# Performance work log

Measured on AMD Instinct MI355X. Metric: run time of the kernel, lower is better.

Reference implementation:

```python
import jax, jax.numpy as jnp
import numpy as np

N, E, NB, P = 100000, 1600000, 1000, 500000


def gcn_conv(x, edge_index, W, b):
    # PyG GCNConv: add self-loops, symmetric D^-1/2 (A+I) D^-1/2 normalization,
    # linear transform, bias.
    n = x.shape[0]
    loop = jnp.arange(n, dtype=edge_index.dtype)
    src = jnp.concatenate([edge_index[0], loop])
    dst = jnp.concatenate([edge_index[1], loop])
    deg = jax.ops.segment_sum(jnp.ones(src.shape[0], x.dtype), dst, num_segments=n)
    dinv = jnp.where(deg > 0, jax.lax.rsqrt(deg), 0.0)
    norm = dinv[src] * dinv[dst]                       # [E+n]
    xw = x @ W                                          # [n, out]
    out = jax.ops.segment_sum(xw[src] * norm[:, None], dst, num_segments=n)
    return out + b


def setup_inputs() -> dict:
    key = jax.random.key(0)
    ks = jax.random.split(key, 12)
    x = jax.random.normal(ks[0], (N, 27), jnp.float32)
    edge_index = jax.random.randint(ks[1], (2, E), 0, N, dtype=jnp.int32)
    bank = jax.random.normal(ks[2], (NB, 27), jnp.float32)
    node1 = jax.random.randint(ks[3], (P,), 0, N + NB, dtype=jnp.int32)
    node2 = jax.random.randint(ks[4], (P,), 0, N + NB, dtype=jnp.int32)

    def lin(k, fan_in, fan_out):
        s = 1.0 / np.sqrt(fan_in)
        kw, kb = jax.random.split(k)
        W = jax.random.uniform(kw, (fan_in, fan_out), jnp.float32, -s, s)
        b = jax.random.uniform(kb, (fan_out,), jnp.float32, -s, s)
        return W, b

    W1, b1 = lin(ks[5], 27, 60)
    W2, b2 = lin(ks[6], 60, 50)
    Wb, bb = lin(ks[7], 27, 50)
    Wf1, bf1 = lin(ks[8], 100, 40)
    Wf2, bf2 = lin(ks[9], 40, 20)
    Wf3, bf3 = lin(ks[10], 20, 4)
    return dict(x=x, bank=bank, W1=W1, b1=b1, W2=W2, b2=b2, Wb=Wb, bb=bb,
                Wf1=Wf1, bf1=bf1, Wf2=Wf2, bf2=bf2, Wf3=Wf3, bf3=bf3,
                edge_index=edge_index, node1=node1, node2=node2)


def reference(x, bank, W1, b1, W2, b2, Wb, bb, Wf1, bf1, Wf2, bf2, Wf3, bf3,
              edge_index, node1, node2):
    h = gcn_conv(x, edge_index, W1, b1)                 # [N, 60]
    h = gcn_conv(h, edge_index, W2, b2)                 # [N, 50]
    bk = bank @ Wb + bb                                 # [NB, 50]
    allh = jnp.concatenate([h, bk], axis=0)             # [N+NB, 50]
    z = jnp.concatenate([allh[node1], allh[node2]], axis=1)  # [P, 100]
    z = z @ Wf1 + bf1
    z = z @ Wf2 + bf2
    z = z @ Wf3 + bf3                                   # [P, 4]
    return jax.nn.softmax(z, axis=0)                    # softmax over dim 0, as in source
```

## Files before the change

### kernel.cpp

```cpp
#include <hip/hip_runtime.h>
#include <math.h>

#define N_NODES 100000
#define N_EDGES 1600000
#define NB_BANK 1000
#define N_PAIRS 500000

#define BUCK_SHIFT 8
#define BUCK_NODES 256
#define NBUCK 391
#define BCAP 5504
#define EPB 4096
#define NSCAT 391
#define NZB4 489
#define SMASK 0x1FFFF

struct Consts {
  float C[27*8];
  float Rb[27*8];
  float u[8];
  float vg[8];
  float vb[8];
};

__device__ void precompute_body(
    const float* __restrict__ W1, const float* __restrict__ b1,
    const float* __restrict__ W2, const float* __restrict__ b2,
    const float* __restrict__ Wb, const float* __restrict__ bb,
    const float* __restrict__ Wf1, const float* __restrict__ bf1,
    const float* __restrict__ Wf2, const float* __restrict__ bf2,
    const float* __restrict__ Wf3, const float* __restrict__ bf3,
    Consts* __restrict__ cst) {
  __shared__ float A[40*4];
  __shared__ float T[100*4];
  __shared__ float B[60*8];
  __shared__ float cvec[4];
  const int tid = threadIdx.x;
  const int nt = blockDim.x;

  for (int idx = tid; idx < 160; idx += nt) {
    int r = idx >> 2, k = idx & 3;
    float s = 0.f;
    for (int j = 0; j < 20; ++j) s += Wf2[r*20+j] * Wf3[j*4+k];
    A[idx] = s;
  }
  __syncthreads();
  for (int idx = tid; idx < 400; idx += nt) {
    int r = idx >> 2, k = idx & 3;
    float s = 0.f;
    for (int j = 0; j < 40; ++j) s += Wf1[r*40+j] * A[j*4+k];
    T[idx] = s;
  }
  if (tid < 4) {
    float s = bf3[tid];
    for (int j = 0; j < 40; ++j) s += bf1[j] * A[j*4+tid];
    for (int j = 0; j < 20; ++j) s += bf2[j] * Wf3[j*4+tid];
    cvec[tid] = s;
  }
  __syncthreads();
  for (int idx = tid; idx < 480; idx += nt) {
    int r = idx >> 3, k = idx & 7;
    int half = k >> 2, kk = k & 3;
    float s = 0.f;
    for (int j = 0; j < 50; ++j) s += W2[r*50+j] * T[(half*50+j)*4+kk];
    B[idx] = s;
  }
  __syncthreads();
  for (int idx = tid; idx < 456; idx += nt) {
    if (idx < 216) {
      int r = idx >> 3, k = idx & 7;
      float s = 0.f;
      for (int j = 0; j < 60; ++j) s += W1[r*60+j] * B[j*8+k];
      cst->C[idx] = s;
    } else if (idx < 432) {
      int i2 = idx - 216;
      int r = i2 >> 3, k = i2 & 7, half = k >> 2, kk = k & 3;
      float s = 0.f;
      for (int j = 0; j < 50; ++j) s += Wb[r*50+j] * T[(half*50+j)*4+kk];
      cst->Rb[i2] = s;
    } else if (idx < 440) {
      int k = idx - 432;
      float s = 0.f;
      for (int j = 0; j < 60; ++j) s += b1[j] * B[j*8+k];
      cst->u[k] = s;
    } else if (idx < 448) {
      int k = idx - 440, half = k >> 2, kk = k & 3;
      float s = (half == 0) ? cvec[kk] : 0.f;
      for (int j = 0; j < 50; ++j) s += b2[j] * T[(half*50+j)*4+kk];
      cst->vg[k] = s;
    } else {
      int k = idx - 448, half = k >> 2, kk = k & 3;
      float s = (half == 0) ? cvec[kk] : 0.f;
      for (int j = 0; j < 50; ++j) s += bb[j] * T[(half*50+j)*4+kk];
      cst->vb[k] = s;
    }
  }
}

__global__ __launch_bounds__(1024) void k_scatter(
    const int* __restrict__ ei, int* __restrict__ bcnt, int* __restrict__ ebuf,
    const float* __restrict__ W1, const float* __restrict__ b1,
    const float* __restrict__ W2, const float* __restrict__ b2,
    const float* __restrict__ Wb, const float* __restrict__ bb,
    const float* __restrict__ Wf1, const float* __restrict__ bf1,
    const float* __restrict__ Wf2, const float* __restrict__ bf2,
    const float* __restrict__ Wf3, const float* __restrict__ bf3,
    Consts* __restrict__ cst) {
  if (blockIdx.x == NSCAT) {
    precompute_body(W1, b1, W2, b2, Wb, bb, Wf1, bf1, Wf2, bf2, Wf3, bf3, cst);
    return;
  }
  __shared__ int hist[NBUCK];
  __shared__ int base[NBUCK];
  const int t = threadIdx.x;
  const int e0 = blockIdx.x * EPB;
  int dcache[EPB / 1024];
  if (t < NBUCK) hist[t] = 0;
  __syncthreads();
#pragma unroll
  for (int i = 0; i < EPB / 1024; ++i) {
    int e = e0 + i * 1024 + t;
    int d = (e < N_EDGES) ? ei[N_EDGES + e] : -1;
    dcache[i] = d;
    if (d >= 0) atomicAdd(&hist[d >> BUCK_SHIFT], 1);
  }
  __syncthreads();
  if (t < NBUCK) {
    int h = hist[t];
    base[t] = h ? (t * BCAP + atomicAdd(&bcnt[t], h)) : 0;
    hist[t] = 0;
  }
  __syncthreads();
#pragma unroll
  for (int i = 0; i < EPB / 1024; ++i) {
    int e = e0 + i * 1024 + t;
    int d = dcache[i];
    if (d >= 0) {
      int s = ei[e];
      int b = d >> BUCK_SHIFT;
      int pos = base[b] + atomicAdd(&hist[b], 1);
      ebuf[pos] = ((d & (BUCK_NODES - 1)) << 17) | s;
    }
  }
}

__global__ __launch_bounds__(512) void k_degfill_x8(
    const int* __restrict__ bcnt, const int* __restrict__ ebuf,
    const float* __restrict__ x, const Consts* __restrict__ cst,
    float* __restrict__ dinv, int* __restrict__ rbeg, int* __restrict__ rend,
    int* __restrict__ csr, float* __restrict__ Xs) {
  __shared__ int cnt[BUCK_NODES];
  __shared__ int lcur[BUCK_NODES];
  __shared__ float sdinv[BUCK_NODES];
  __shared__ float xs[BUCK_NODES * 27];
  const int b = blockIdx.x;
  const int t = threadIdx.x;
  if (t < BUCK_NODES) cnt[t] = 0;
  __syncthreads();
  const int beg = b * BCAP, end = beg + bcnt[b];
  for (int j = beg + t; j < end; j += 512)
    atomicAdd(&cnt[ebuf[j] >> 17], 1);
  const int xbase = b * (BUCK_NODES * 27);
  for (int j = t; j < BUCK_NODES * 27; j += 512) {
    int g = xbase + j;
    xs[j] = (g < N_NODES * 27) ? x[g] : 0.f;
  }
  __syncthreads();
  int v = (t < BUCK_NODES) ? cnt[t] : 0;
  for (int off = 1; off < BUCK_NODES; off <<= 1) {
    int u = (t < BUCK_NODES && t >= off) ? cnt[t - off] : 0;
    __syncthreads();
    if (t < BUCK_NODES) cnt[t] += u;
    __syncthreads();
  }
  if (t < BUCK_NODES) {
    const int node = (b << BUCK_SHIFT) + t;
    const int excl = beg + cnt[t] - v;
    lcur[t] = excl;
    float dv = rsqrtf((float)v + 1.0f);
    sdinv[t] = dv;
    if (node < N_NODES) {
      rbeg[node] = excl;
      rend[node] = excl + v;
      dinv[node] = dv;
    }
  }
  __syncthreads();
  for (int j = beg + t; j < end; j += 512) {
    int code = ebuf[j];
    int pos = atomicAdd(&lcur[code >> 17], 1);
    csr[pos] = code & SMASK;
  }
  for (int idx = t; idx < BUCK_NODES * 8; idx += 512) {
    int li = idx >> 3, k = idx & 7;
    int node = (b << BUCK_SHIFT) + li;
    if (node < N_NODES) {
      float s = 0.f;
      for (int c = 0; c < 27; ++c) s += xs[li*27+c] * cst->C[c*8+k];
      Xs[(size_t)node*8+k] = s * sdinv[li];
    }
  }
}

__global__ __launch_bounds__(256) void k_gather1(const int* __restrict__ rbeg,
                                                 const int* __restrict__ rend,
                                                 const int* __restrict__ csr,
                                                 const float* __restrict__ dinv,
                                                 const float2* __restrict__ Xs2,
                                                 float2* __restrict__ Ys2,
                                                 float* __restrict__ dvec) {
  int t = blockIdx.x * 256 + threadIdx.x;
  int d = t >> 2, q = t & 3;
  if (d >= N_NODES) return;
  const int beg = rbeg[d], end = rend[d];
  const float nd = dinv[d];
  float2 self = Xs2[d*4 + q];
  float ax = self.x, ay = self.y;
  float dsum = nd;
  int j = beg;
  if (j + 8 <= end) {
    int s0 = csr[j],   s1 = csr[j+1], s2 = csr[j+2], s3 = csr[j+3];
    int s4 = csr[j+4], s5 = csr[j+5], s6 = csr[j+6], s7 = csr[j+7];
    for (;;) {
      float2 a0 = Xs2[s0*4+q], a1 = Xs2[s1*4+q], a2 = Xs2[s2*4+q], a3 = Xs2[s3*4+q];
      float2 a4 = Xs2[s4*4+q], a5 = Xs2[s5*4+q], a6 = Xs2[s6*4+q], a7 = Xs2[s7*4+q];
      float d0 = 0.f, d1 = 0.f, d2 = 0.f, d3 = 0.f;
      float d4 = 0.f, d5 = 0.f, d6 = 0.f, d7 = 0.f;
      if (q == 0) {
        d0 = dinv[s0]; d1 = dinv[s1]; d2 = dinv[s2]; d3 = dinv[s3];
        d4 = dinv[s4]; d5 = dinv[s5]; d6 = dinv[s6]; d7 = dinv[s7];
      }
      int jn = j + 8;
      bool more = (jn + 8 <= end);
      int u0, u1, u2, u3, u4, u5, u6, u7;
      if (more) {
        u0 = csr[jn];   u1 = csr[jn+1]; u2 = csr[jn+2]; u3 = csr[jn+3];
        u4 = csr[jn+4]; u5 = csr[jn+5]; u6 = csr[jn+6]; u7 = csr[jn+7];
      } else {
        u0 = u1 = u2 = u3 = u4 = u5 = u6 = u7 = 0;
      }
      ax += ((a0.x + a1.x) + (a2.x + a3.x)) + ((a4.x + a5.x) + (a6.x + a7.x));
      ay += ((a0.y + a1.y) + (a2.y + a3.y)) + ((a4.y + a5.y) + (a6.y + a7.y));
      if (q == 0)
        dsum += ((d0 + d1) + (d2 + d3)) + ((d4 + d5) + (d6 + d7));
      j = jn;
      if (!more) break;
      s0 = u0; s1 = u1; s2 = u2; s3 = u3;
      s4 = u4; s5 = u5; s6 = u6; s7 = u7;
    }
  }
  if (j + 4 <= end) {
    int a = csr[j], b = csr[j+1], c = csr[j+2], e = csr[j+3];
    float2 p0 = Xs2[a*4+q], p1 = Xs2[b*4+q], p2 = Xs2[c*4+q], p3 = Xs2[e*4+q];
    ax += (p0.x + p1.x) + (p2.x + p3.x);
    ay += (p0.y + p1.y) + (p2.y + p3.y);
    if (q == 0) dsum += (dinv[a] + dinv[b]) + (dinv[c] + dinv[e]);
    j += 4;
  }
  for (; j < end; ++j) {
    int s = csr[j];
    float2 a = Xs2[s*4+q];
    ax += a.x; ay += a.y;
    if (q == 0) dsum += dinv[s];
  }
  float nn = nd * nd;
  Ys2[t] = make_float2(nn * ax, nn * ay);
  if (q == 0) dvec[d] = nd * dsum;
}

__global__ __launch_bounds__(256) void k_gather2g(const int* __restrict__ rbeg,
                                                  const int* __restrict__ rend,
                                                  const int* __restrict__ csr,
                                                  const float* __restrict__ dinv,
                                                  const float2* __restrict__ Ys2,
                                                  const float* __restrict__ dvec,
                                                  const float* __restrict__ bank,
                                                  const Consts* __restrict__ cst,
                                                  float2* __restrict__ gall2) {
  int t = blockIdx.x * 256 + threadIdx.x;
  int d = t >> 2, q = t & 3;
  if (d >= N_NODES + NB_BANK) return;
  int c0 = 2*q, c1 = 2*q + 1;
  if (d >= N_NODES) {
    int bk = d - N_NODES;
    float sx = cst->vb[c0], sy = cst->vb[c1];
    for (int cc = 0; cc < 27; ++cc) {
      float bv = bank[bk*27+cc];
      sx += bv * cst->Rb[cc*8+c0];
      sy += bv * cst->Rb[cc*8+c1];
    }
    gall2[t] = make_float2(sx, sy);
    return;
  }
  const int beg = rbeg[d], end = rend[d];
  float2 self = Ys2[d*4 + q];
  float ax = self.x, ay = self.y;
  int j = beg;
  if (j + 8 <= end) {
    int s0 = csr[j],   s1 = csr[j+1], s2 = csr[j+2], s3 = csr[j+3];
    int s4 = csr[j+4], s5 = csr[j+5], s6 = csr[j+6], s7 = csr[j+7];
    for (;;) {
      float2 a0 = Ys2[s0*4+q], a1 = Ys2[s1*4+q], a2 = Ys2[s2*4+q], a3 = Ys2[s3*4+q];
      float2 a4 = Ys2[s4*4+q], a5 = Ys2[s5*4+q], a6 = Ys2[s6*4+q], a7 = Ys2[s7*4+q];
      int jn = j + 8;
      bool more = (jn + 8 <= end);
      int u0, u1, u2, u3, u4, u5, u6, u7;
      if (more) {
        u0 = csr[jn];   u1 = csr[jn+1]; u2 = csr[jn+2]; u3 = csr[jn+3];
        u4 = csr[jn+4]; u5 = csr[jn+5]; u6 = csr[jn+6]; u7 = csr[jn+7];
      } else {
        u0 = u1 = u2 = u3 = u4 = u5 = u6 = u7 = 0;
      }
      ax += ((a0.x + a1.x) + (a2.x + a3.x)) + ((a4.x + a5.x) + (a6.x + a7.x));
      ay += ((a0.y + a1.y) + (a2.y + a3.y)) + ((a4.y + a5.y) + (a6.y + a7.y));
      j = jn;
      if (!more) break;
      s0 = u0; s1 = u1; s2 = u2; s3 = u3;
      s4 = u4; s5 = u5; s6 = u6; s7 = u7;
    }
  }
  if (j + 4 <= end) {
    int a = csr[j], b = csr[j+1], c = csr[j+2], e = csr[j+3];
    float2 p0 = Ys2[a*4+q], p1 = Ys2[b*4+q], p2 = Ys2[c*4+q], p3 = Ys2[e*4+q];
    ax += (p0.x + p1.x) + (p2.x + p3.x);
    ay += (p0.y + p1.y) + (p2.y + p3.y);
    j += 4;
  }
  for (; j < end; ++j) {
    float2 a = Ys2[csr[j]*4+q];
    ax += a.x; ay += a.y;
  }
  float nd = dinv[d], dv = dvec[d];
  gall2[t] = make_float2(nd * ax + dv * cst->u[c0] + cst->vg[c0],
                         nd * ay + dv * cst->u[c1] + cst->vg[c1]);
}

__device__ inline void sm_merge(float4& m1, float4& s1,
                                const float4 m2, const float4 s2) {
  float4 M;
  M.x = fmaxf(m1.x, m2.x); M.y = fmaxf(m1.y, m2.y);
  M.z = fmaxf(m1.z, m2.z); M.w = fmaxf(m1.w, m2.w);
  s1.x = s1.x * expf(m1.x - M.x) + s2.x * expf(m2.x - M.x);
  s1.y = s1.y * expf(m1.y - M.y) + s2.y * expf(m2.y - M.y);
  s1.z = s1.z * expf(m1.z - M.z) + s2.z * expf(m2.z - M.z);
  s1.w = s1.w * expf(m1.w - M.w) + s2.w * expf(m2.w - M.w);
  m1 = M;
}

__global__ __launch_bounds__(256) void k_z(const int* __restrict__ node1,
                                           const int* __restrict__ node2,
                                           const float* __restrict__ gall,
                                           float4* __restrict__ bs_m,
                                           float4* __restrict__ bs_s) {
  const int S = NZB4 * 256;
  int p0 = blockIdx.x * 256 + threadIdx.x;
  float4 m = make_float4(-1e30f, -1e30f, -1e30f, -1e30f);
  float4 s = make_float4(0.f, 0.f, 0.f, 0.f);
#pragma unroll
  for (int i = 0; i < 4; ++i) {
    int p = p0 + i * S;
    if (p < N_PAIRS) {
      int n1 = node1[p], n2 = node2[p];
      const float4 a = *(const float4*)(gall + (size_t)n1*8);
      const float4 b = *(const float4*)(gall + (size_t)n2*8 + 4);
      float4 zv = make_float4(a.x+b.x, a.y+b.y, a.z+b.z, a.w+b.w);
      sm_merge(m, s, zv, make_float4(1.f, 1.f, 1.f, 1.f));
    }
  }
  __shared__ float4 lm[256], ls[256];
  lm[threadIdx.x] = m; ls[threadIdx.x] = s;
  __syncthreads();
  for (int st = 128; st > 0; st >>= 1) {
    if (threadIdx.x < st) {
      float4 mm = lm[threadIdx.x], ss = ls[threadIdx.x];
      sm_merge(mm, ss, lm[threadIdx.x + st], ls[threadIdx.x + st]);
      lm[threadIdx.x] = mm; ls[threadIdx.x] = ss;
    }
    __syncthreads();
  }
  if (threadIdx.x == 0) { bs_m[blockIdx.x] = lm[0]; bs_s[blockIdx.x] = ls[0]; }
}

__global__ __launch_bounds__(256) void k_final(const int* __restrict__ node1,
                                               const int* __restrict__ node2,
                                               const float* __restrict__ gall,
                                               const float4* __restrict__ bs_m,
                                               const float4* __restrict__ bs_s,
                                               float* __restrict__ out) {
  float4 m = make_float4(-1e30f, -1e30f, -1e30f, -1e30f);
  float4 s = make_float4(0.f, 0.f, 0.f, 0.f);
  for (int i = threadIdx.x; i < NZB4; i += 256)
    sm_merge(m, s, bs_m[i], bs_s[i]);
  __shared__ float4 lm[256], ls[256];
  lm[threadIdx.x] = m; ls[threadIdx.x] = s;
  __syncthreads();
  for (int st = 128; st > 0; st >>= 1) {
    if (threadIdx.x < st) {
      float4 mm = lm[threadIdx.x], ss = ls[threadIdx.x];
      sm_merge(mm, ss, lm[threadIdx.x + st], ls[threadIdx.x + st]);
      lm[threadIdx.x] = mm; ls[threadIdx.x] = ss;
    }
    __syncthreads();
  }
  const float4 M = lm[0], S4 = ls[0];
  const float i0 = 1.f / S4.x, i1 = 1.f / S4.y;
  const float i2 = 1.f / S4.z, i3 = 1.f / S4.w;
  const int S = NZB4 * 256;
  int p0 = blockIdx.x * 256 + threadIdx.x;
#pragma unroll
  for (int i = 0; i < 4; ++i) {
    int p = p0 + i * S;
    if (p < N_PAIRS) {
      int n1 = node1[p], n2 = node2[p];
      const float4 a = *(const float4*)(gall + (size_t)n1*8);
      const float4 b = *(const float4*)(gall + (size_t)n2*8 + 4);
      float4 zv = make_float4(a.x+b.x, a.y+b.y, a.z+b.z, a.w+b.w);
      float4 o = make_float4(expf(zv.x - M.x) * i0, expf(zv.y - M.y) * i1,
                             expf(zv.z - M.z) * i2, expf(zv.w - M.w) * i3);
      ((float4*)out)[p] = o;
    }
  }
}

extern "C" void kernel_launch(void* const* d_in, const int* in_sizes, int n_in,
                              void* d_out, int out_size, void* d_ws, size_t ws_size,
                              hipStream_t stream) {
  const float* x    = (const float*)d_in[0];
  const float* bank = (const float*)d_in[1];
  const float* W1   = (const float*)d_in[2];
  const float* b1   = (const float*)d_in[3];
  const float* W2   = (const float*)d_in[4];
  const float* b2   = (const float*)d_in[5];
  const float* Wb   = (const float*)d_in[6];
  const float* bb   = (const float*)d_in[7];
  const float* Wf1  = (const float*)d_in[8];
  const float* bf1  = (const float*)d_in[9];
  const float* Wf2  = (const float*)d_in[10];
  const float* bf2  = (const float*)d_in[11];
  const float* Wf3  = (const float*)d_in[12];
  const float* bf3  = (const float*)d_in[13];
  const int* ei     = (const int*)d_in[14];
  const int* node1  = (const int*)d_in[15];
  const int* node2  = (const int*)d_in[16];
  float* out = (float*)d_out;

  char* w = (char*)d_ws;
  size_t off = 0;
  auto take = [&](size_t bytes) -> char* {
    char* p = w + off;
    off = (off + bytes + 255) & ~(size_t)255;
    return p;
  };
  Consts* cst    = (Consts*)take(sizeof(Consts));
  int*    bcnt   = (int*)take(NBUCK * 4);
  float*  dinv   = (float*)take(N_NODES * 4);
  int*    rbeg   = (int*)take(N_NODES * 4);
  int*    rend   = (int*)take(N_NODES * 4);
  int*    csr    = (int*)take((size_t)NBUCK * BCAP * 4);
  float*  Xs     = (float*)take((size_t)N_NODES * 8 * 4);
  float*  Ys     = (float*)take((size_t)N_NODES * 8 * 4);
  float*  dvec   = (float*)take(N_NODES * 4);
  float*  gall   = (float*)take((size_t)(N_NODES + NB_BANK) * 8 * 4);
  int*    ebuf   = (int*)take((size_t)NBUCK * BCAP * 4);
  float4* bs_m   = (float4*)take((size_t)NZB4 * 16);
  float4* bs_s   = (float4*)take((size_t)NZB4 * 16);

  hipMemsetAsync(bcnt, 0, NBUCK * 4, stream);

  k_scatter<<<NSCAT + 1, 1024, 0, stream>>>(ei, bcnt, ebuf, W1, b1, W2, b2,
                                            Wb, bb, Wf1, bf1, Wf2, bf2,
                                            Wf3, bf3, cst);
  k_degfill_x8<<<NBUCK, 512, 0, stream>>>(bcnt, ebuf, x, cst,
                                          dinv, rbeg, rend, csr, Xs);
  k_gather1<<<(N_NODES * 4 + 255) / 256, 256, 0, stream>>>(
      rbeg, rend, csr, dinv, (const float2*)Xs, (float2*)Ys, dvec);
  k_gather2g<<<((N_NODES + NB_BANK) * 4 + 255) / 256, 256, 0, stream>>>(
      rbeg, rend, csr, dinv, (const float2*)Ys, dvec, bank, cst, (float2*)gall);
  k_z<<<NZB4, 256, 0, stream>>>(node1, node2, gall, bs_m, bs_s);
  k_final<<<NZB4, 256, 0, stream>>>(node1, node2, gall, bs_m, bs_s, out);
}
```

Baseline: 202.2 us.

## Fuse all stages into one persistent cooperative kernel with grid syncs

Replaces the six separate launches (scatter, degree/fill, two gathers, softmax partials, final) with one cooperative kernel that runs each stage in grid-stride loops and separates them with grid.sync(). Shared memory is reused across stages through a union. The goal is to remove per-launch overhead and inter-kernel gaps. In exchange, parallelism is capped at the resident block count (at most 512 blocks of 512 threads), grid-wide barriers add their own cost, and each stage loses the per-kernel tuned block shapes.

```diff
diff --git a/kernel.cpp b/kernel.cpp
--- a/kernel.cpp
+++ b/kernel.cpp
@@ -1,5 +1,8 @@
 #include <hip/hip_runtime.h>
+#include <hip/hip_cooperative_groups.h>
 #include <math.h>
+
+namespace cg = cooperative_groups;
 
 #define N_NODES 100000
 #define N_EDGES 1600000
@@ -12,8 +15,9 @@
 #define BCAP 5504
 #define EPB 4096
 #define NSCAT 391
-#define NZB4 489
 #define SMASK 0x1FFFF
+#define NTH 512
+#define MAXB 512
 
 struct Consts {
   float C[27*8];
@@ -23,21 +27,31 @@
   float vb[8];
 };
 
-__device__ void precompute_body(
-    const float* __restrict__ W1, const float* __restrict__ b1,
-    const float* __restrict__ W2, const float* __restrict__ b2,
-    const float* __restrict__ Wb, const float* __restrict__ bb,
-    const float* __restrict__ Wf1, const float* __restrict__ bf1,
-    const float* __restrict__ Wf2, const float* __restrict__ bf2,
-    const float* __restrict__ Wf3, const float* __restrict__ bf3,
-    Consts* __restrict__ cst) {
-  __shared__ float A[40*4];
-  __shared__ float T[100*4];
-  __shared__ float B[60*8];
-  __shared__ float cvec[4];
-  const int tid = threadIdx.x;
-  const int nt = blockDim.x;
-
+struct P {
+  const float *x, *bank, *W1, *b1, *W2, *b2, *Wb, *bb;
+  const float *Wf1, *bf1, *Wf2, *bf2, *Wf3, *bf3;
+  const int *ei, *node1, *node2;
+  float* out;
+  Consts* cst;
+  int* bcnt; float* dinv; int* rbeg; int* rend; int* csr;
+  float* Xs; float* Ys; float* dvec; float* gall;
+  int* ebuf; float4* bs_m; float4* bs_s;
+};
+
+union ShU {
+  struct { int hist[NBUCK]; int base[NBUCK]; } sc;
+  struct { float A[40*4]; float T[100*4]; float Bm[60*8]; float cvec[4]; } pc;
+  struct { int cnt[BUCK_NODES]; int lcur[BUCK_NODES];
+           float sdinv[BUCK_NODES]; float xs[BUCK_NODES*27]; } df;
+  struct { float4 lm[NTH]; float4 ls[NTH]; } pr;
+};
+
+__device__ void precompute_body(const P& prm, float* A, float* T, float* Bm,
+                                float* cvec, int tid, int nt) {
+  const float *W1 = prm.W1, *b1 = prm.b1, *W2 = prm.W2, *b2 = prm.b2;
+  const float *Wb = prm.Wb, *bb = prm.bb, *Wf1 = prm.Wf1, *bf1 = prm.bf1;
+  const float *Wf2 = prm.Wf2, *bf2 = prm.bf2, *Wf3 = prm.Wf3, *bf3 = prm.bf3;
+  Consts* cst = prm.cst;
   for (int idx = tid; idx < 160; idx += nt) {
     int r = idx >> 2, k = idx & 3;
     float s = 0.f;
@@ -63,14 +77,14 @@
     int half = k >> 2, kk = k & 3;
     float s = 0.f;
     for (int j = 0; j < 50; ++j) s += W2[r*50+j] * T[(half*50+j)*4+kk];
-    B[idx] = s;
+    Bm[idx] = s;
   }
   __syncthreads();
   for (int idx = tid; idx < 456; idx += nt) {
     if (idx < 216) {
       int r = idx >> 3, k = idx & 7;
       float s = 0.f;
-      for (int j = 0; j < 60; ++j) s += W1[r*60+j] * B[j*8+k];
+      for (int j = 0; j < 60; ++j) s += W1[r*60+j] * Bm[j*8+k];
       cst->C[idx] = s;
     } else if (idx < 432) {
       int i2 = idx - 216;
@@ -81,7 +95,7 @@
     } else if (idx < 440) {
       int k = idx - 432;
       float s = 0.f;
-      for (int j = 0; j < 60; ++j) s += b1[j] * B[j*8+k];
+      for (int j = 0; j < 60; ++j) s += b1[j] * Bm[j*8+k];
       cst->u[k] = s;
     } else if (idx < 448) {
       int k = idx - 440, half = k >> 2, kk = k & 3;
@@ -97,244 +111,6 @@
   }
 }
 
-__global__ __launch_bounds__(1024) void k_scatter(
-    const int* __restrict__ ei, int* __restrict__ bcnt, int* __restrict__ ebuf,
-    const float* __restrict__ W1, const float* __restrict__ b1,
-    const float* __restrict__ W2, const float* __restrict__ b2,
-    const float* __restrict__ Wb, const float* __restrict__ bb,
-    const float* __restrict__ Wf1, const float* __restrict__ bf1,
-    const float* __restrict__ Wf2, const float* __restrict__ bf2,
-    const float* __restrict__ Wf3, const float* __restrict__ bf3,
-    Consts* __restrict__ cst) {
-  if (blockIdx.x == NSCAT) {
-    precompute_body(W1, b1, W2, b2, Wb, bb, Wf1, bf1, Wf2, bf2, Wf3, bf3, cst);
-    return;
-  }
-  __shared__ int hist[NBUCK];
-  __shared__ int base[NBUCK];
-  const int t = threadIdx.x;
-  const int e0 = blockIdx.x * EPB;
-  int dcache[EPB / 1024];
-  if (t < NBUCK) hist[t] = 0;
-  __syncthreads();
-#pragma unroll
-  for (int i = 0; i < EPB / 1024; ++i) {
-    int e = e0 + i * 1024 + t;
-    int d = (e < N_EDGES) ? ei[N_EDGES + e] : -1;
-    dcache[i] = d;
-    if (d >= 0) atomicAdd(&hist[d >> BUCK_SHIFT], 1);
-  }
-  __syncthreads();
-  if (t < NBUCK) {
-    int h = hist[t];
-    base[t] = h ? (t * BCAP + atomicAdd(&bcnt[t], h)) : 0;
-    hist[t] = 0;
-  }
-  __syncthreads();
-#pragma unroll
-  for (int i = 0; i < EPB / 1024; ++i) {
-    int e = e0 + i * 1024 + t;
-    int d = dcache[i];
-    if (d >= 0) {
-      int s = ei[e];
-      int b = d >> BUCK_SHIFT;
-      int pos = base[b] + atomicAdd(&hist[b], 1);
-      ebuf[pos] = ((d & (BUCK_NODES - 1)) << 17) | s;
-    }
-  }
-}
-
-__global__ __launch_bounds__(512) void k_degfill_x8(
-    const int* __restrict__ bcnt, const int* __restrict__ ebuf,
-    const float* __restrict__ x, const Consts* __restrict__ cst,
-    float* __restrict__ dinv, int* __restrict__ rbeg, int* __restrict__ rend,
-    int* __restrict__ csr, float* __restrict__ Xs) {
-  __shared__ int cnt[BUCK_NODES];
-  __shared__ int lcur[BUCK_NODES];
-  __shared__ float sdinv[BUCK_NODES];
-  __shared__ float xs[BUCK_NODES * 27];
-  const int b = blockIdx.x;
-  const int t = threadIdx.x;
-  if (t < BUCK_NODES) cnt[t] = 0;
-  __syncthreads();
-  const int beg = b * BCAP, end = beg + bcnt[b];
-  for (int j = beg + t; j < end; j += 512)
-    atomicAdd(&cnt[ebuf[j] >> 17], 1);
-  const int xbase = b * (BUCK_NODES * 27);
-  for (int j = t; j < BUCK_NODES * 27; j += 512) {
-    int g = xbase + j;
-    xs[j] = (g < N_NODES * 27) ? x[g] : 0.f;
-  }
-  __syncthreads();
-  int v = (t < BUCK_NODES) ? cnt[t] : 0;
-  for (int off = 1; off < BUCK_NODES; off <<= 1) {
-    int u = (t < BUCK_NODES && t >= off) ? cnt[t - off] : 0;
-    __syncthreads();
-    if (t < BUCK_NODES) cnt[t] += u;
-    __syncthreads();
-  }
-  if (t < BUCK_NODES) {
-    const int node = (b << BUCK_SHIFT) + t;
-    const int excl = beg + cnt[t] - v;
-    lcur[t] = excl;
-    float dv = rsqrtf((float)v + 1.0f);
-    sdinv[t] = dv;
-    if (node < N_NODES) {
-      rbeg[node] = excl;
-      rend[node] = excl + v;
-      dinv[node] = dv;
-    }
-  }
-  __syncthreads();
-  for (int j = beg + t; j < end; j += 512) {
-    int code = ebuf[j];
-    int pos = atomicAdd(&lcur[code >> 17], 1);
-    csr[pos] = code & SMASK;
-  }
-  for (int idx = t; idx < BUCK_NODES * 8; idx += 512) {
-    int li = idx >> 3, k = idx & 7;
-    int node = (b << BUCK_SHIFT) + li;
-    if (node < N_NODES) {
-      float s = 0.f;
-      for (int c = 0; c < 27; ++c) s += xs[li*27+c] * cst->C[c*8+k];
-      Xs[(size_t)node*8+k] = s * sdinv[li];
-    }
-  }
-}
-
-__global__ __launch_bounds__(256) void k_gather1(const int* __restrict__ rbeg,
-                                                 const int* __restrict__ rend,
-                                                 const int* __restrict__ csr,
-                                                 const float* __restrict__ dinv,
-                                                 const float2* __restrict__ Xs2,
-                                                 float2* __restrict__ Ys2,
-                                                 float* __restrict__ dvec) {
-  int t = blockIdx.x * 256 + threadIdx.x;
-  int d = t >> 2, q = t & 3;
-  if (d >= N_NODES) return;
-  const int beg = rbeg[d], end = rend[d];
-  const float nd = dinv[d];
-  float2 self = Xs2[d*4 + q];
-  float ax = self.x, ay = self.y;
-  float dsum = nd;
-  int j = beg;
-  if (j + 8 <= end) {
-    int s0 = csr[j],   s1 = csr[j+1], s2 = csr[j+2], s3 = csr[j+3];
-    int s4 = csr[j+4], s5 = csr[j+5], s6 = csr[j+6], s7 = csr[j+7];
-    for (;;) {
-      float2 a0 = Xs2[s0*4+q], a1 = Xs2[s1*4+q], a2 = Xs2[s2*4+q], a3 = Xs2[s3*4+q];
-      float2 a4 = Xs2[s4*4+q], a5 = Xs2[s5*4+q], a6 = Xs2[s6*4+q], a7 = Xs2[s7*4+q];
-      float d0 = 0.f, d1 = 0.f, d2 = 0.f, d3 = 0.f;
-      float d4 = 0.f, d5 = 0.f, d6 = 0.f, d7 = 0.f;
-      if (q == 0) {
-        d0 = dinv[s0]; d1 = dinv[s1]; d2 = dinv[s2]; d3 = dinv[s3];
-        d4 = dinv[s4]; d5 = dinv[s5]; d6 = dinv[s6]; d7 = dinv[s7];
-      }
-      int jn = j + 8;
-      bool more = (jn + 8 <= end);
-      int u0, u1, u2, u3, u4, u5, u6, u7;
-      if (more) {
-        u0 = csr[jn];   u1 = csr[jn+1]; u2 = csr[jn+2]; u3 = csr[jn+3];
-        u4 = csr[jn+4]; u5 = csr[jn+5]; u6 = csr[jn+6]; u7 = csr[jn+7];
-      } else {
-        u0 = u1 = u2 = u3 = u4 = u5 = u6 = u7 = 0;
-      }
-      ax += ((a0.x + a1.x) + (a2.x + a3.x)) + ((a4.x + a5.x) + (a6.x + a7.x));
-      ay += ((a0.y + a1.y) + (a2.y + a3.y)) + ((a4.y + a5.y) + (a6.y + a7.y));
-      if (q == 0)
-        dsum += ((d0 + d1) + (d2 + d3)) + ((d4 + d5) + (d6 + d7));
-      j = jn;
-      if (!more) break;
-      s0 = u0; s1 = u1; s2 = u2; s3 = u3;
-      s4 = u4; s5 = u5; s6 = u6; s7 = u7;
-    }
-  }
-  if (j + 4 <= end) {
-    int a = csr[j], b = csr[j+1], c = csr[j+2], e = csr[j+3];
-    float2 p0 = Xs2[a*4+q], p1 = Xs2[b*4+q], p2 = Xs2[c*4+q], p3 = Xs2[e*4+q];
-    ax += (p0.x + p1.x) + (p2.x + p3.x);
-    ay += (p0.y + p1.y) + (p2.y + p3.y);
-    if (q == 0) dsum += (dinv[a] + dinv[b]) + (dinv[c] + dinv[e]);
-    j += 4;
-  }
-  for (; j < end; ++j) {
-    int s = csr[j];
-    float2 a = Xs2[s*4+q];
-    ax += a.x; ay += a.y;
-    if (q == 0) dsum += dinv[s];
-  }
-  float nn = nd * nd;
-  Ys2[t] = make_float2(nn * ax, nn * ay);
-  if (q == 0) dvec[d] = nd * dsum;
-}
-
-__global__ __launch_bounds__(256) void k_gather2g(const int* __restrict__ rbeg,
-                                                  const int* __restrict__ rend,
-                                                  const int* __restrict__ csr,
-                                                  const float* __restrict__ dinv,
-                                                  const float2* __restrict__ Ys2,
-                                                  const float* __restrict__ dvec,
-                                                  const float* __restrict__ bank,
-                                                  const Consts* __restrict__ cst,
-                                                  float2* __restrict__ gall2) {
-  int t = blockIdx.x * 256 + threadIdx.x;
-  int d = t >> 2, q = t & 3;
-  if (d >= N_NODES + NB_BANK) return;
-  int c0 = 2*q, c1 = 2*q + 1;
-  if (d >= N_NODES) {
-    int bk = d - N_NODES;
-    float sx = cst->vb[c0], sy = cst->vb[c1];
-    for (int cc = 0; cc < 27; ++cc) {
-      float bv = bank[bk*27+cc];
-      sx += bv * cst->Rb[cc*8+c0];
-      sy += bv * cst->Rb[cc*8+c1];
-    }
-    gall2[t] = make_float2(sx, sy);
-    return;
-  }
-  const int beg = rbeg[d], end = rend[d];
-  float2 self = Ys2[d*4 + q];
-  float ax = self.x, ay = self.y;
-  int j = beg;
-  if (j + 8 <= end) {
-    int s0 = csr[j],   s1 = csr[j+1], s2 = csr[j+2], s3 = csr[j+3];
-    int s4 = csr[j+4], s5 = csr[j+5], s6 = csr[j+6], s7 = csr[j+7];
-    for (;;) {
-      float2 a0 = Ys2[s0*4+q], a1 = Ys2[s1*4+q], a2 = Ys2[s2*4+q], a3 = Ys2[s3*4+q];
-      float2 a4 = Ys2[s4*4+q], a5 = Ys2[s5*4+q], a6 = Ys2[s6*4+q], a7 = Ys2[s7*4+q];
-      int jn = j + 8;
-      bool more = (jn + 8 <= end);
-      int u0, u1, u2, u3, u4, u5, u6, u7;
-      if (more) {
-        u0 = csr[jn];   u1 = csr[jn+1]; u2 = csr[jn+2]; u3 = csr[jn+3];
-        u4 = csr[jn+4]; u5 = csr[jn+5]; u6 = csr[jn+6]; u7 = csr[jn+7];
-      } else {
-        u0 = u1 = u2 = u3 = u4 = u5 = u6 = u7 = 0;
-      }
-      ax += ((a0.x + a1.x) + (a2.x + a3.x)) + ((a4.x + a5.x) + (a6.x + a7.x));
-      ay += ((a0.y + a1.y) + (a2.y + a3.y)) + ((a4.y + a5.y) + (a6.y + a7.y));
-      j = jn;
-      if (!more) break;
-      s0 = u0; s1 = u1; s2 = u2; s3 = u3;
-      s4 = u4; s5 = u5; s6 = u6; s7 = u7;
-    }
-  }
-  if (j + 4 <= end) {
-    int a = csr[j], b = csr[j+1], c = csr[j+2], e = csr[j+3];
-    float2 p0 = Ys2[a*4+q], p1 = Ys2[b*4+q], p2 = Ys2[c*4+q], p3 = Ys2[e*4+q];
-    ax += (p0.x + p1.x) + (p2.x + p3.x);
-    ay += (p0.y + p1.y) + (p2.y + p3.y);
-    j += 4;
-  }
-  for (; j < end; ++j) {
-    float2 a = Ys2[csr[j]*4+q];
-    ax += a.x; ay += a.y;
-  }
-  float nd = dinv[d], dv = dvec[d];
-  gall2[t] = make_float2(nd * ax + dv * cst->u[c0] + cst->vg[c0],
-                         nd * ay + dv * cst->u[c1] + cst->vg[c1]);
-}
-
 __device__ inline void sm_merge(float4& m1, float4& s1,
                                 const float4 m2, const float4 s2) {
   float4 M;
@@ -347,77 +123,280 @@
   m1 = M;
 }
 
-__global__ __launch_bounds__(256) void k_z(const int* __restrict__ node1,
-                                           const int* __restrict__ node2,
-                                           const float* __restrict__ gall,
-                                           float4* __restrict__ bs_m,
-                                           float4* __restrict__ bs_s) {
-  const int S = NZB4 * 256;
-  int p0 = blockIdx.x * 256 + threadIdx.x;
-  float4 m = make_float4(-1e30f, -1e30f, -1e30f, -1e30f);
-  float4 s = make_float4(0.f, 0.f, 0.f, 0.f);
+__device__ void gather1_body(int t, const P& prm) {
+  const float2* Xs2 = (const float2*)prm.Xs;
+  int d = t >> 2, q = t & 3;
+  const int beg = prm.rbeg[d], end = prm.rend[d];
+  const float nd = prm.dinv[d];
+  float2 self = Xs2[d*4 + q];
+  float ax = self.x, ay = self.y;
+  float dsum = nd;
+  int j = beg;
+  if (j + 8 <= end) {
+    int s0 = prm.csr[j],   s1 = prm.csr[j+1], s2 = prm.csr[j+2], s3 = prm.csr[j+3];
+    int s4 = prm.csr[j+4], s5 = prm.csr[j+5], s6 = prm.csr[j+6], s7 = prm.csr[j+7];
+    for (;;) {
+      float2 a0 = Xs2[s0*4+q], a1 = Xs2[s1*4+q], a2 = Xs2[s2*4+q], a3 = Xs2[s3*4+q];
+      float2 a4 = Xs2[s4*4+q], a5 = Xs2[s5*4+q], a6 = Xs2[s6*4+q], a7 = Xs2[s7*4+q];
+      float d0 = 0.f, d1 = 0.f, d2 = 0.f, d3 = 0.f;
+      float d4 = 0.f, d5 = 0.f, d6 = 0.f, d7 = 0.f;
+      if (q == 0) {
+        d0 = prm.dinv[s0]; d1 = prm.dinv[s1]; d2 = prm.dinv[s2]; d3 = prm.dinv[s3];
+        d4 = prm.dinv[s4]; d5 = prm.dinv[s5]; d6 = prm.dinv[s6]; d7 = prm.dinv[s7];
+      }
+      int jn = j + 8;
+      bool more = (jn + 8 <= end);
+      int u0, u1, u2, u3, u4, u5, u6, u7;
+      if (more) {
+        u0 = prm.csr[jn];   u1 = prm.csr[jn+1]; u2 = prm.csr[jn+2]; u3 = prm.csr[jn+3];
+        u4 = prm.csr[jn+4]; u5 = prm.csr[jn+5]; u6 = prm.csr[jn+6]; u7 = prm.csr[jn+7];
+      } else {
+        u0 = u1 = u2 = u3 = u4 = u5 = u6 = u7 = 0;
+      }
+      ax += ((a0.x + a1.x) + (a2.x + a3.x)) + ((a4.x + a5.x) + (a6.x + a7.x));
+      ay += ((a0.y + a1.y) + (a2.y + a3.y)) + ((a4.y + a5.y) + (a6.y + a7.y));
+      if (q == 0)
+        dsum += ((d0 + d1) + (d2 + d3)) + ((d4 + d5) + (d6 + d7));
+      j = jn;
+      if (!more) break;
+      s0 = u0; s1 = u1; s2 = u2; s3 = u3;
+      s4 = u4; s5 = u5; s6 = u6; s7 = u7;
+    }
+  }
+  if (j + 4 <= end) {
+    int a = prm.csr[j], b = prm.csr[j+1], c = prm.csr[j+2], e = prm.csr[j+3];
+    float2 p0 = Xs2[a*4+q], p1 = Xs2[b*4+q], p2 = Xs2[c*4+q], p3 = Xs2[e*4+q];
+    ax += (p0.x + p1.x) + (p2.x + p3.x);
+    ay += (p0.y + p1.y) + (p2.y + p3.y);
+    if (q == 0) dsum += (prm.dinv[a] + prm.dinv[b]) + (prm.dinv[c] + prm.dinv[e]);
+    j += 4;
+  }
+  for (; j < end; ++j) {
+    int s = prm.csr[j];
+    float2 a = Xs2[s*4+q];
+    ax += a.x; ay += a.y;
+    if (q == 0) dsum += prm.dinv[s];
+  }
+  float nn = nd * nd;
+  ((float2*)prm.Ys)[t] = make_float2(nn * ax, nn * ay);
+  if (q == 0) prm.dvec[d] = nd * dsum;
+}
+
+__device__ void gather2_body(int t, const P& prm) {
+  const float2* Ys2 = (const float2*)prm.Ys;
+  float2* gall2 = (float2*)prm.gall;
+  int d = t >> 2, q = t & 3;
+  int c0 = 2*q, c1 = 2*q + 1;
+  if (d >= N_NODES) {
+    int bk = d - N_NODES;
+    float sx = prm.cst->vb[c0], sy = prm.cst->vb[c1];
+    for (int cc = 0; cc < 27; ++cc) {
+      float bv = prm.bank[bk*27+cc];
+      sx += bv * prm.cst->Rb[cc*8+c0];
+      sy += bv * prm.cst->Rb[cc*8+c1];
+    }
+    gall2[t] = make_float2(sx, sy);
+    return;
+  }
+  const int beg = prm.rbeg[d], end = prm.rend[d];
+  float2 self = Ys2[d*4 + q];
+  float ax = self.x, ay = self.y;
+  int j = beg;
+  if (j + 8 <= end) {
+    int s0 = prm.csr[j],   s1 = prm.csr[j+1], s2 = prm.csr[j+2], s3 = prm.csr[j+3];
+    int s4 = prm.csr[j+4], s5 = prm.csr[j+5], s6 = prm.csr[j+6], s7 = prm.csr[j+7];
+    for (;;) {
+      float2 a0 = Ys2[s0*4+q], a1 = Ys2[s1*4+q], a2 = Ys2[s2*4+q], a3 = Ys2[s3*4+q];
+      float2 a4 = Ys2[s4*4+q], a5 = Ys2[s5*4+q], a6 = Ys2[s6*4+q], a7 = Ys2[s7*4+q];
+      int jn = j + 8;
+      bool more = (jn + 8 <= end);
+      int u0, u1, u2, u3, u4, u5, u6, u7;
+      if (more) {
+        u0 = prm.csr[jn];   u1 = prm.csr[jn+1]; u2 = prm.csr[jn+2]; u3 = prm.csr[jn+3];
+        u4 = prm.csr[jn+4]; u5 = prm.csr[jn+5]; u6 = prm.csr[jn+6]; u7 = prm.csr[jn+7];
+      } else {
+        u0 = u1 = u2 = u3 = u4 = u5 = u6 = u7 = 0;
+      }
+      ax += ((a0.x + a1.x) + (a2.x + a3.x)) + ((a4.x + a5.x) + (a6.x + a7.x));
+      ay += ((a0.y + a1.y) + (a2.y + a3.y)) + ((a4.y + a5.y) + (a6.y + a7.y));
+      j = jn;
+      if (!more) break;
+      s0 = u0; s1 = u1; s2 = u2; s3 = u3;
+      s4 = u4; s5 = u5; s6 = u6; s7 = u7;
+    }
+  }
+  if (j + 4 <= end) {
+    int a = prm.csr[j], b = prm.csr[j+1], c = prm.csr[j+2], e = prm.csr[j+3];
+    float2 p0 = Ys2[a*4+q], p1 = Ys2[b*4+q], p2 = Ys2[c*4+q], p3 = Ys2[e*4+q];
+    ax += (p0.x + p1.x) + (p2.x + p3.x);
+    ay += (p0.y + p1.y) + (p2.y + p3.y);
+    j += 4;
+  }
+  for (; j < end; ++j) {
+    float2 a = Ys2[prm.csr[j]*4+q];
+    ax += a.x; ay += a.y;
+  }
+  float nd = prm.dinv[d], dv = prm.dvec[d];
+  gall2[t] = make_float2(nd * ax + dv * prm.cst->u[c0] + prm.cst->vg[c0],
+                         nd * ay + dv * prm.cst->u[c1] + prm.cst->vg[c1]);
+}
+
+__global__ __launch_bounds__(NTH, 4) void k_fused(P prm) {
+  cg::grid_group grid = cg::this_grid();
+  __shared__ ShU sh;
+  const int p  = threadIdx.x;
+  const int B  = blockIdx.x;
+  const int NB = gridDim.x;
+  const int GT = NB * NTH;
+  const int g  = B * NTH + p;
+
+  if (B == 0)
+    for (int i = p; i < NBUCK; i += NTH) prm.bcnt[i] = 0;
+  grid.sync();
+
+  if (B == NB - 1) {
+    precompute_body(prm, sh.pc.A, sh.pc.T, sh.pc.Bm, sh.pc.cvec, p, NTH);
+  } else {
+    for (int c = B; c < NSCAT; c += NB - 1) {
+      for (int i = p; i < NBUCK; i += NTH) sh.sc.hist[i] = 0;
+      __syncthreads();
+      int dcache[EPB / NTH];
 #pragma unroll
-  for (int i = 0; i < 4; ++i) {
-    int p = p0 + i * S;
-    if (p < N_PAIRS) {
-      int n1 = node1[p], n2 = node2[p];
-      const float4 a = *(const float4*)(gall + (size_t)n1*8);
-      const float4 b = *(const float4*)(gall + (size_t)n2*8 + 4);
+      for (int i = 0; i < EPB / NTH; ++i) {
+        int e = c * EPB + i * NTH + p;
+        int d = (e < N_EDGES) ? prm.ei[N_EDGES + e] : -1;
+        dcache[i] = d;
+        if (d >= 0) atomicAdd(&sh.sc.hist[d >> BUCK_SHIFT], 1);
+      }
+      __syncthreads();
+      for (int i = p; i < NBUCK; i += NTH) {
+        int h = sh.sc.hist[i];
+        sh.sc.base[i] = h ? (i * BCAP + atomicAdd(&prm.bcnt[i], h)) : 0;
+        sh.sc.hist[i] = 0;
+      }
+      __syncthreads();
+#pragma unroll
+      for (int i = 0; i < EPB / NTH; ++i) {
+        int e = c * EPB + i * NTH + p;
+        int d = dcache[i];
+        if (d >= 0) {
+          int s = prm.ei[e];
+          int bb2 = d >> BUCK_SHIFT;
+          int pos = sh.sc.base[bb2] + atomicAdd(&sh.sc.hist[bb2], 1);
+          prm.ebuf[pos] = ((d & (BUCK_NODES - 1)) << 17) | s;
+        }
+      }
+      __syncthreads();
+    }
+  }
+  grid.sync();
+
+  for (int b = B; b < NBUCK; b += NB) {
+    if (p < BUCK_NODES) sh.df.cnt[p] = 0;
+    __syncthreads();
+    const int beg = b * BCAP, end = beg + prm.bcnt[b];
+    for (int j = beg + p; j < end; j += NTH)
+      atomicAdd(&sh.df.cnt[prm.ebuf[j] >> 17], 1);
+    const int xbase = b * (BUCK_NODES * 27);
+    for (int j = p; j < BUCK_NODES * 27; j += NTH) {
+      int gx = xbase + j;
+      sh.df.xs[j] = (gx < N_NODES * 27) ? prm.x[gx] : 0.f;
+    }
+    __syncthreads();
+    int v = (p < BUCK_NODES) ? sh.df.cnt[p] : 0;
+    for (int off = 1; off < BUCK_NODES; off <<= 1) {
+      int u = (p < BUCK_NODES && p >= off) ? sh.df.cnt[p - off] : 0;
+      __syncthreads();
+      if (p < BUCK_NODES) sh.df.cnt[p] += u;
+      __syncthreads();
+    }
+    if (p < BUCK_NODES) {
+      const int node = (b << BUCK_SHIFT) + p;
+      const int excl = beg + sh.df.cnt[p] - v;
+      sh.df.lcur[p] = excl;
+      float dv = rsqrtf((float)v + 1.0f);
+      sh.df.sdinv[p] = dv;
+      if (node < N_NODES) {
+        prm.rbeg[node] = excl;
+        prm.rend[node] = excl + v;
+        prm.dinv[node] = dv;
+      }
+    }
+    __syncthreads();
+    for (int j = beg + p; j < end; j += NTH) {
+      int code = prm.ebuf[j];
+      int pos = atomicAdd(&sh.df.lcur[code >> 17], 1);
+      prm.csr[pos] = code & SMASK;
+    }
+    for (int idx = p; idx < BUCK_NODES * 8; idx += NTH) {
+      int li = idx >> 3, k = idx & 7;
+      int node = (b << BUCK_SHIFT) + li;
+      if (node < N_NODES) {
+        float s = 0.f;
+        for (int c = 0; c < 27; ++c) s += sh.df.xs[li*27+c] * prm.cst->C[c*8+k];
+        prm.Xs[(size_t)node*8+k] = s * sh.df.sdinv[li];
+      }
+    }
+    __syncthreads();
+  }
+  grid.sync();
+
+  for (int t = g; t < N_NODES * 4; t += GT) gather1_body(t, prm);
+  grid.sync();
+
+  for (int t = g; t < (N_NODES + NB_BANK) * 4; t += GT) gather2_body(t, prm);
+  grid.sync();
+
+  {
+    float4 m = make_float4(-1e30f, -1e30f, -1e30f, -1e30f);
+    float4 s = make_float4(0.f, 0.f, 0.f, 0.f);
+    for (int pp = g; pp < N_PAIRS; pp += GT) {
+      int n1 = prm.node1[pp], n2 = prm.node2[pp];
+      const float4 a = *(const float4*)(prm.gall + (size_t)n1*8);
+      const float4 b = *(const float4*)(prm.gall + (size_t)n2*8 + 4);
       float4 zv = make_float4(a.x+b.x, a.y+b.y, a.z+b.z, a.w+b.w);
       sm_merge(m, s, zv, make_float4(1.f, 1.f, 1.f, 1.f));
     }
-  }
-  __shared__ float4 lm[256], ls[256];
-  lm[threadIdx.x] = m; ls[threadIdx.x] = s;
-  __syncthreads();
-  for (int st = 128; st > 0; st >>= 1) {
-    if (threadIdx.x < st) {
-      float4 mm = lm[threadIdx.x], ss = ls[threadIdx.x];
-      sm_merge(mm, ss, lm[threadIdx.x + st], ls[threadIdx.x + st]);
-      lm[threadIdx.x] = mm; ls[threadIdx.x] = ss;
-    }
-    __syncthreads();
-  }
-  if (threadIdx.x == 0) { bs_m[blockIdx.x] = lm[0]; bs_s[blockIdx.x] = ls[0]; }
-}
-
-__global__ __launch_bounds__(256) void k_final(const int* __restrict__ node1,
-                                               const int* __restrict__ node2,
-                                               const float* __restrict__ gall,
-                                               const float4* __restrict__ bs_m,
-                                               const float4* __restrict__ bs_s,
-                                               float* __restrict__ out) {
-  float4 m = make_float4(-1e30f, -1e30f, -1e30f, -1e30f);
-  float4 s = make_float4(0.f, 0.f, 0.f, 0.f);
-  for (int i = threadIdx.x; i < NZB4; i += 256)
-    sm_merge(m, s, bs_m[i], bs_s[i]);
-  __shared__ float4 lm[256], ls[256];
-  lm[threadIdx.x] = m; ls[threadIdx.x] = s;
-  __syncthreads();
-  for (int st = 128; st > 0; st >>= 1) {
-    if (threadIdx.x < st) {
-      float4 mm = lm[threadIdx.x], ss = ls[threadIdx.x];
-      sm_merge(mm, ss, lm[threadIdx.x + st], ls[threadIdx.x + st]);
-      lm[threadIdx.x] = mm; ls[threadIdx.x] = ss;
-    }
-    __syncthreads();
-  }
-  const float4 M = lm[0], S4 = ls[0];
-  const float i0 = 1.f / S4.x, i1 = 1.f / S4.y;
-  const float i2 = 1.f / S4.z, i3 = 1.f / S4.w;
-  const int S = NZB4 * 256;
-  int p0 = blockIdx.x * 256 + threadIdx.x;
-#pragma unroll
-  for (int i = 0; i < 4; ++i) {
-    int p = p0 + i * S;
-    if (p < N_PAIRS) {
-      int n1 = node1[p], n2 = node2[p];
-      const float4 a = *(const float4*)(gall + (size_t)n1*8);
-      const float4 b = *(const float4*)(gall + (size_t)n2*8 + 4);
+    sh.pr.lm[p] = m; sh.pr.ls[p] = s;
+    __syncthreads();
+    for (int st = NTH / 2; st > 0; st >>= 1) {
+      if (p < st) {
+        float4 mm = sh.pr.lm[p], ss = sh.pr.ls[p];
+        sm_merge(mm, ss, sh.pr.lm[p + st], sh.pr.ls[p + st]);
+        sh.pr.lm[p] = mm; sh.pr.ls[p] = ss;
+      }
+      __syncthreads();
+    }
+    if (p == 0) { prm.bs_m[B] = sh.pr.lm[0]; prm.bs_s[B] = sh.pr.ls[0]; }
+  }
+  grid.sync();
+
+  {
+    float4 m = make_float4(-1e30f, -1e30f, -1e30f, -1e30f);
+    float4 s = make_float4(0.f, 0.f, 0.f, 0.f);
+    for (int i = p; i < NB; i += NTH)
+      sm_merge(m, s, prm.bs_m[i], prm.bs_s[i]);
+    sh.pr.lm[p] = m; sh.pr.ls[p] = s;
+    __syncthreads();
+    for (int st = NTH / 2; st > 0; st >>= 1) {
+      if (p < st) {
+        float4 mm = sh.pr.lm[p], ss = sh.pr.ls[p];
+        sm_merge(mm, ss, sh.pr.lm[p + st], sh.pr.ls[p + st]);
+        sh.pr.lm[p] = mm; sh.pr.ls[p] = ss;
+      }
+      __syncthreads();
+    }
+    const float4 M = sh.pr.lm[0], S4 = sh.pr.ls[0];
+    const float i0 = 1.f / S4.x, i1 = 1.f / S4.y;
+    const float i2 = 1.f / S4.z, i3 = 1.f / S4.w;
+    for (int pp = g; pp < N_PAIRS; pp += GT) {
+      int n1 = prm.node1[pp], n2 = prm.node2[pp];
+      const float4 a = *(const float4*)(prm.gall + (size_t)n1*8);
+      const float4 b = *(const float4*)(prm.gall + (size_t)n2*8 + 4);
       float4 zv = make_float4(a.x+b.x, a.y+b.y, a.z+b.z, a.w+b.w);
       float4 o = make_float4(expf(zv.x - M.x) * i0, expf(zv.y - M.y) * i1,
                              expf(zv.z - M.z) * i2, expf(zv.w - M.w) * i3);
-      ((float4*)out)[p] = o;
+      ((float4*)prm.out)[pp] = o;
     }
   }
 }
@@ -425,57 +404,58 @@
 extern "C" void kernel_launch(void* const* d_in, const int* in_sizes, int n_in,
                               void* d_out, int out_size, void* d_ws, size_t ws_size,
                               hipStream_t stream) {
-  const float* x    = (const float*)d_in[0];
-  const float* bank = (const float*)d_in[1];
-  const float* W1   = (const float*)d_in[2];
-  const float* b1   = (const float*)d_in[3];
-  const float* W2   = (const float*)d_in[4];
-  const float* b2   = (const float*)d_in[5];
-  const float* Wb   = (const float*)d_in[6];
-  const float* bb   = (const float*)d_in[7];
-  const float* Wf1  = (const float*)d_in[8];
-  const float* bf1  = (const float*)d_in[9];
-  const float* Wf2  = (const float*)d_in[10];
-  const float* bf2  = (const float*)d_in[11];
-  const float* Wf3  = (const float*)d_in[12];
-  const float* bf3  = (const float*)d_in[13];
-  const int* ei     = (const int*)d_in[14];
-  const int* node1  = (const int*)d_in[15];
-  const int* node2  = (const int*)d_in[16];
-  float* out = (float*)d_out;
-
   char* w = (char*)d_ws;
   size_t off = 0;
   auto take = [&](size_t bytes) -> char* {
-    char* p = w + off;
+    char* pp = w + off;
     off = (off + bytes + 255) & ~(size_t)255;
-    return p;
+    return pp;
   };
-  Consts* cst    = (Consts*)take(sizeof(Consts));
-  int*    bcnt   = (int*)take(NBUCK * 4);
-  float*  dinv   = (float*)take(N_NODES * 4);
-  int*    rbeg   = (int*)take(N_NODES * 4);
-  int*    rend   = (int*)take(N_NODES * 4);
-  int*    csr    = (int*)take((size_t)NBUCK * BCAP * 4);
-  float*  Xs     = (float*)take((size_t)N_NODES * 8 * 4);
-  float*  Ys     = (float*)take((size_t)N_NODES * 8 * 4);
-  float*  dvec   = (float*)take(N_NODES * 4);
-  float*  gall   = (float*)take((size_t)(N_NODES + NB_BANK) * 8 * 4);
-  int*    ebuf   = (int*)take((size_t)NBUCK * BCAP * 4);
-  float4* bs_m   = (float4*)take((size_t)NZB4 * 16);
-  float4* bs_s   = (float4*)take((size_t)NZB4 * 16);
-
-  hipMemsetAsync(bcnt, 0, NBUCK * 4, stream);
-
-  k_scatter<<<NSCAT + 1, 1024, 0, stream>>>(ei, bcnt, ebuf, W1, b1, W2, b2,
-                                            Wb, bb, Wf1, bf1, Wf2, bf2,
-                                            Wf3, bf3, cst);
-  k_degfill_x8<<<NBUCK, 512, 0, stream>>>(bcnt, ebuf, x, cst,
-                                          dinv, rbeg, rend, csr, Xs);
-  k_gather1<<<(N_NODES * 4 + 255) / 256, 256, 0, stream>>>(
-      rbeg, rend, csr, dinv, (const float2*)Xs, (float2*)Ys, dvec);
-  k_gather2g<<<((N_NODES + NB_BANK) * 4 + 255) / 256, 256, 0, stream>>>(
-      rbeg, rend, csr, dinv, (const float2*)Ys, dvec, bank, cst, (float2*)gall);
-  k_z<<<NZB4, 256, 0, stream>>>(node1, node2, gall, bs_m, bs_s);
-  k_final<<<NZB4, 256, 0, stream>>>(node1, node2, gall, bs_m, bs_s, out);
-}
+  P prm;
+  prm.x    = (const float*)d_in[0];
+  prm.bank = (const float*)d_in[1];
+  prm.W1   = (const float*)d_in[2];
+  prm.b1   = (const float*)d_in[3];
+  prm.W2   = (const float*)d_in[4];
+  prm.b2   = (const float*)d_in[5];
+  prm.Wb   = (const float*)d_in[6];
+  prm.bb   = (const float*)d_in[7];
+  prm.Wf1  = (const float*)d_in[8];
+  prm.bf1  = (const float*)d_in[9];
+  prm.Wf2  = (const float*)d_in[10];
+  prm.bf2  = (const float*)d_in[11];
+  prm.Wf3  = (const float*)d_in[12];
+  prm.bf3  = (const float*)d_in[13];
+  prm.ei   = (const int*)d_in[14];
+  prm.node1 = (const int*)d_in[15];
+  prm.node2 = (const int*)d_in[16];
+  prm.out  = (float*)d_out;
+
+  prm.cst  = (Consts*)take(sizeof(Consts));
+  prm.bcnt = (int*)take(NBUCK * 4);
+  prm.dinv = (float*)take(N_NODES * 4);
+  prm.rbeg = (int*)take(N_NODES * 4);
+  prm.rend = (int*)take(N_NODES * 4);
+  prm.csr  = (int*)take((size_t)NBUCK * BCAP * 4);
+  prm.Xs   = (float*)take((size_t)N_NODES * 8 * 4);
+  prm.Ys   = (float*)take((size_t)N_NODES * 8 * 4);
+  prm.dvec = (float*)take(N_NODES * 4);
+  prm.gall = (float*)take((size_t)(N_NODES + NB_BANK) * 8 * 4);
+  prm.ebuf = (int*)take((size_t)NBUCK * BCAP * 4);
+  prm.bs_m = (float4*)take((size_t)MAXB * 16);
+  prm.bs_s = (float4*)take((size_t)MAXB * 16);
+
+  static int nblk = 0;
+  if (nblk == 0) {
+    int maxb = 0;
+    hipOccupancyMaxActiveBlocksPerMultiprocessor(&maxb, k_fused, NTH, 0);
+    if (maxb < 1) maxb = 1;
+    nblk = maxb * 256;
+    if (nblk > MAXB) nblk = MAXB;
+    if (nblk < 2) nblk = 2;
+  }
+
+  void* args[] = { (void*)&prm };
+  hipLaunchCooperativeKernel((const void*)k_fused, dim3(nblk), dim3(NTH),
+                             args, 0, stream);
+}
```

Measured after the change: 406.0 us. 2.01x slower.
